# Performance work log

Hardware: AMD Instinct MI355X
Metric: run time of the kernel (lower is better)

## Reference

```python
import jax, jax.numpy as jnp
import numpy as np

KERNEL_SIZE = 3
ITERATIONS = 4


def _box_conv(x, kernel):
    # x: [B,1,H,W], kernel: [1,1,k,k]; SAME padding via pad=(k-1)//2
    p = (KERNEL_SIZE - 1) // 2
    return jax.lax.conv_general_dilated(
        x, kernel,
        window_strides=(1, 1),
        padding=((p, p), (p, p)),
        dimension_numbers=("NCHW", "OIHW", "NCHW"),
    )


def setup_inputs() -> dict:
    key = jax.random.key(0)
    inputs = jax.random.uniform(key, (32, 1, 512, 512), dtype=jnp.float32)
    return {"inputs": inputs}


def reference(inputs) -> jnp.ndarray:
    # fixed box-filter kernel: every tap = 1/k^2, bias = 0 (frozen in torch module)
    kernel = jnp.full((1, 1, KERNEL_SIZE, KERNEL_SIZE), 1.0 / KERNEL_SIZE**2, dtype=inputs.dtype)
    blob = inputs
    for _ in range(ITERATIONS):
        # NOTE: original module convolves `inputs` (not previous blob) each iteration
        blob = _box_conv(inputs, kernel)
        blob = jax.nn.sigmoid((blob - 0.01) * 1000.0)
        blob = _box_conv(blob, kernel)
        blob = jax.nn.sigmoid((blob - 0.9) * 1000.0)
    return blob
```

## Files before the change

kernel.cpp:

```cpp
#include <hip/hip_runtime.h>


#define IMG 512
#define BH  4
#define NR  (BH + 4)
#define NIT (BH + 2)

__device__ __forceinline__ float steep_sig(float sum9, float bias) {
    float x = fmaf(sum9, 1000.0f / 9.0f, bias);
    return __builtin_amdgcn_rcpf(1.0f + __expf(-x));
}

__device__ __forceinline__ float4 f4add3(float4 a, float4 b, float4 c) {
    return make_float4(a.x + b.x + c.x, a.y + b.y + c.y,
                       a.z + b.z + c.z, a.w + b.w + c.w);
}

__global__ __launch_bounds__(256, 4) void blobber_fused(const float* __restrict__ in,
                                                        float* __restrict__ out) {
    const int tid  = threadIdx.x;
    const int lane = tid & 63;
    const int gw   = blockIdx.x * 4 + (tid >> 6);
    const int band = gw & 127;
    const int img  = gw >> 7;
    const int y0   = band * BH;
    const int xA   = 8 * lane;

    const float* ip = in  + (size_t)img * (IMG * IMG);
    float*       op = out + (size_t)img * (IMG * IMG);

    float4 A[NR], B[NR];
    #pragma unroll
    for (int k = 0; k < NR; ++k) {
        const int r = y0 - 2 + k;
        A[k] = make_float4(0.f, 0.f, 0.f, 0.f);
        B[k] = make_float4(0.f, 0.f, 0.f, 0.f);
        if ((unsigned)r < IMG) {
            const float* row = ip + r * IMG + xA;
            A[k] = *(const float4*)(row);
            B[k] = *(const float4*)(row + 4);
        }
    }

    const float4 z4 = make_float4(0.f, 0.f, 0.f, 0.f);
    float4 h2mA = z4, h2mB = z4, h2cA = z4, h2cB = z4;

    #pragma unroll
    for (int s = 0; s < NIT; ++s) {
        const int r = y0 - 1 + s;

        float4 vA = f4add3(A[s], A[s + 1], A[s + 2]);
        float4 vB = f4add3(B[s], B[s + 1], B[s + 2]);

        float lft = __shfl_up(vB.w, 1);
        float rgt = __shfl_down(vA.x, 1);
        if (lane == 0)  lft = 0.0f;
        if (lane == 63) rgt = 0.0f;

        float4 s1A, s1B;
        if ((unsigned)r < IMG) {
            s1A.x = steep_sig(lft  + vA.x + vA.y, -10.0f);
            s1A.y = steep_sig(vA.x + vA.y + vA.z, -10.0f);
            s1A.z = steep_sig(vA.y + vA.z + vA.w, -10.0f);
            s1A.w = steep_sig(vA.z + vA.w + vB.x, -10.0f);
            s1B.x = steep_sig(vA.w + vB.x + vB.y, -10.0f);
            s1B.y = steep_sig(vB.x + vB.y + vB.z, -10.0f);
            s1B.z = steep_sig(vB.y + vB.z + vB.w, -10.0f);
            s1B.w = steep_sig(vB.z + vB.w + rgt,  -10.0f);
        } else {
            s1A = z4; s1B = z4;
        }

        float slft = __shfl_up(s1B.w, 1);
        float srgt = __shfl_down(s1A.x, 1);
        if (lane == 0)  slft = 0.0f;
        if (lane == 63) srgt = 0.0f;

        float4 h2pA, h2pB;
        h2pA.x = slft  + s1A.x + s1A.y;
        h2pA.y = s1A.x + s1A.y + s1A.z;
        h2pA.z = s1A.y + s1A.z + s1A.w;
        h2pA.w = s1A.z + s1A.w + s1B.x;
        h2pB.x = s1A.w + s1B.x + s1B.y;
        h2pB.y = s1B.x + s1B.y + s1B.z;
        h2pB.z = s1B.y + s1B.z + s1B.w;
        h2pB.w = s1B.z + s1B.w + srgt;

        if (s >= 2) {
            const int oy = r - 1;
            float4 oA, oB;
            oA.x = steep_sig(h2mA.x + h2cA.x + h2pA.x, -900.0f);
            oA.y = steep_sig(h2mA.y + h2cA.y + h2pA.y, -900.0f);
            oA.z = steep_sig(h2mA.z + h2cA.z + h2pA.z, -900.0f);
            oA.w = steep_sig(h2mA.w + h2cA.w + h2pA.w, -900.0f);
            oB.x = steep_sig(h2mB.x + h2cB.x + h2pB.x, -900.0f);
            oB.y = steep_sig(h2mB.y + h2cB.y + h2pB.y, -900.0f);
            oB.z = steep_sig(h2mB.z + h2cB.z + h2pB.z, -900.0f);
            oB.w = steep_sig(h2mB.w + h2cB.w + h2pB.w, -900.0f);
            float* orow = op + oy * IMG + xA;
            *(float4*)(orow)     = oA;
            *(float4*)(orow + 4) = oB;
        }

        h2mA = h2cA; h2mB = h2cB;
        h2cA = h2pA; h2cB = h2pB;
    }
}

extern "C" void kernel_launch(void* const* d_in, const int* in_sizes, int n_in,
                              void* d_out, int out_size, void* d_ws, size_t ws_size,
                              hipStream_t stream) {
    const float* in  = (const float*)d_in[0];
    float*       out = (float*)d_out;
    blobber_fused<<<dim3(1024), dim3(256), 0, stream>>>(in, out);
}
```

Before: 84.11 us.

## Double band height per wave and stream input rows through a rolling register window

Each wavefront now processes an 8-row band instead of 4, which halves the redundant halo row loads (4 extra rows per band) and halves the grid to 512 blocks. Input rows are no longer preloaded all at once. A rolling 4-row register window is prefetched one row ahead per iteration, which keeps register use bounded despite the taller band. The cost is fewer waves in flight (2048 waves on the device) and a more serial dependency chain per wave, which may lower latency hiding.

```diff
diff --git a/kernel.cpp b/kernel.cpp
--- a/kernel.cpp
+++ b/kernel.cpp
@@ -2,8 +2,7 @@
 
 
 #define IMG 512
-#define BH  4
-#define NR  (BH + 4)
+#define BH  8
 #define NIT (BH + 2)
 
 __device__ __forceinline__ float steep_sig(float sum9, float bias) {
@@ -21,36 +20,43 @@
     const int tid  = threadIdx.x;
     const int lane = tid & 63;
     const int gw   = blockIdx.x * 4 + (tid >> 6);
-    const int band = gw & 127;
-    const int img  = gw >> 7;
+    const int band = gw & 63;
+    const int img  = gw >> 6;
     const int y0   = band * BH;
     const int xA   = 8 * lane;
 
     const float* ip = in  + (size_t)img * (IMG * IMG);
     float*       op = out + (size_t)img * (IMG * IMG);
 
-    float4 A[NR], B[NR];
-    #pragma unroll
-    for (int k = 0; k < NR; ++k) {
-        const int r = y0 - 2 + k;
-        A[k] = make_float4(0.f, 0.f, 0.f, 0.f);
-        B[k] = make_float4(0.f, 0.f, 0.f, 0.f);
-        if ((unsigned)r < IMG) {
+    const int lastRow = y0 + BH + 1;
+    const float4 z4 = make_float4(0.f, 0.f, 0.f, 0.f);
+
+    auto loadRow = [&](int r, float4& a, float4& b) {
+        a = z4; b = z4;
+        if ((unsigned)r < IMG && r <= lastRow) {
             const float* row = ip + r * IMG + xA;
-            A[k] = *(const float4*)(row);
-            B[k] = *(const float4*)(row + 4);
+            a = *(const float4*)(row);
+            b = *(const float4*)(row + 4);
         }
-    }
+    };
 
-    const float4 z4 = make_float4(0.f, 0.f, 0.f, 0.f);
+    float4 bA, bB, cA, cB, dA, dB, eA, eB;
+    loadRow(y0 - 2, bA, bB);
+    loadRow(y0 - 1, cA, cB);
+    loadRow(y0,     dA, dB);
+    loadRow(y0 + 1, eA, eB);
+
     float4 h2mA = z4, h2mB = z4, h2cA = z4, h2cB = z4;
 
     #pragma unroll
     for (int s = 0; s < NIT; ++s) {
         const int r = y0 - 1 + s;
 
-        float4 vA = f4add3(A[s], A[s + 1], A[s + 2]);
-        float4 vB = f4add3(B[s], B[s + 1], B[s + 2]);
+        float4 fA, fB;
+        loadRow(r + 3, fA, fB);
+
+        float4 vA = f4add3(bA, cA, dA);
+        float4 vB = f4add3(bB, cB, dB);
 
         float lft = __shfl_up(vB.w, 1);
         float rgt = __shfl_down(vA.x, 1);
@@ -104,6 +110,10 @@
 
         h2mA = h2cA; h2mB = h2cB;
         h2cA = h2pA; h2cB = h2pB;
+        bA = cA; bB = cB;
+        cA = dA; cB = dB;
+        dA = eA; dB = eB;
+        eA = fA; eB = fB;
     }
 }
 
@@ -112,5 +122,5 @@
                               hipStream_t stream) {
     const float* in  = (const float*)d_in[0];
     float*       out = (float*)d_out;
-    blobber_fused<<<dim3(1024), dim3(256), 0, stream>>>(in, out);
+    blobber_fused<<<dim3(512), dim3(256), 0, stream>>>(in, out);
 }
```

New measurement: 84.95 us. Within noise of the previous version (+1.0%).
